# Kernel optimization log

Measured on AMD Instinct MI355X. Metric: run time of the kernel, lower is better.

The kernel has to match this reference:

```python
import jax, jax.numpy as jnp
import numpy as np

N_NODES = 50000
N_EDGES = 1600000
IN_DIM, HID_DIM, OUT_DIM = 512, 512, 256
K = 10        # APPNP propagation steps (num_layers)
ALPHA = 0.2   # teleport probability


def setup_inputs() -> dict:
    key = jax.random.key(0)
    ks = jax.random.split(key, 8)
    x = jax.random.normal(ks[0], (N_NODES, IN_DIM), dtype=jnp.float32)
    edge_index = jax.random.randint(ks[1], (2, N_EDGES), 0, N_NODES, dtype=jnp.int32)
    # Glorot-ish init for linear weights
    W1 = jax.random.normal(ks[2], (IN_DIM, HID_DIM), dtype=jnp.float32) / np.sqrt(IN_DIM)
    b1 = jnp.zeros((HID_DIM,), dtype=jnp.float32)
    W2 = jax.random.normal(ks[3], (HID_DIM, HID_DIM), dtype=jnp.float32) / np.sqrt(HID_DIM)
    b2 = jnp.zeros((HID_DIM,), dtype=jnp.float32)
    W3 = jax.random.normal(ks[4], (HID_DIM, OUT_DIM), dtype=jnp.float32) / np.sqrt(HID_DIM)
    b3 = jnp.zeros((OUT_DIM,), dtype=jnp.float32)
    return {"x": x, "edge_index": edge_index, "W1": W1, "b1": b1,
            "W2": W2, "b2": b2, "W3": W3, "b3": b3}


def reference(x, edge_index, W1, b1, W2, b2, W3, b3):
    n = x.shape[0]
    # MLP encoder (dropout is identity in inference mode)
    h = jax.nn.relu(x @ W1 + b1)
    h = jax.nn.relu(h @ W2 + b2)
    h = h @ W3 + b3
    # GCN symmetric normalization with self-loops (PyG gcn_norm)
    self_loops = jnp.arange(n, dtype=edge_index.dtype)
    src = jnp.concatenate([edge_index[0], self_loops])  # message sources j
    dst = jnp.concatenate([edge_index[1], self_loops])  # aggregation targets i
    deg = jax.ops.segment_sum(jnp.ones_like(src, dtype=h.dtype), dst, num_segments=n)
    dinv = jnp.where(deg > 0, jax.lax.rsqrt(jnp.maximum(deg, 1.0)), 0.0)
    norm = (dinv[src] * dinv[dst])[:, None]  # [E+N, 1]
    # APPNP: h <- (1-alpha) * A_hat @ h + alpha * h0, K times
    h0 = h
    for _ in range(K):
        agg = jax.ops.segment_sum(h[src] * norm, dst, num_segments=n)
        h = (1.0 - ALPHA) * agg + ALPHA * h0
    return h
```

## Files before the change

### kernel.cpp

```cpp
#include <hip/hip_runtime.h>
#include <hip/hip_bf16.h>
#include <stdint.h>

#define ALPHA_F 0.2f
#define K_STEPS 10

typedef __attribute__((ext_vector_type(8))) short short8;
typedef __attribute__((ext_vector_type(4))) float f32x4;
typedef __attribute__((ext_vector_type(4))) unsigned short u16x4;
typedef __attribute__((ext_vector_type(2))) int i32x2;

__device__ __forceinline__ float bf2f(unsigned short u) {
  union { unsigned int i; float f; } v; v.i = ((unsigned int)u) << 16; return v.f;
}
__device__ __forceinline__ unsigned short f2bf(float f) {
  unsigned int x = __float_as_uint(f);
  unsigned int r = (x + 0x7fffu + ((x >> 16) & 1u)) >> 16;
  return (unsigned short)r;
}

__device__ __forceinline__ void glds16(const void* g, void* l) {
  __builtin_amdgcn_global_load_lds(
      (const __attribute__((address_space(1))) void*)g,
      (__attribute__((address_space(3))) void*)l, 16, 0, 0);
}


__global__ void k_init_deg(int* __restrict__ deg, int n) {
  int i = blockIdx.x * blockDim.x + threadIdx.x;
  if (i < n) deg[i] = 1;
}

__global__ void k_hist(const int* __restrict__ dst, int* __restrict__ deg, int E) {
  int e = blockIdx.x * blockDim.x + threadIdx.x;
  if (e < E) atomicAdd(&deg[dst[e]], 1);
}

__global__ void k_scan(const int* __restrict__ counts, int* __restrict__ rowptr, int n) {
  __shared__ int tmp[1024];
  __shared__ int carry_s;
  const int tid = threadIdx.x;
  if (tid == 0) carry_s = 0;
  __syncthreads();
  for (int base = 0; base < n; base += 1024) {
    int idx = base + tid;
    int v = (idx < n) ? counts[idx] : 0;
    tmp[tid] = v;
    __syncthreads();
    #pragma unroll
    for (int off = 1; off < 1024; off <<= 1) {
      int t = (tid >= off) ? tmp[tid - off] : 0;
      __syncthreads();
      tmp[tid] += t;
      __syncthreads();
    }
    int c = carry_s;
    if (idx < n) rowptr[idx] = c + tmp[tid] - v;
    __syncthreads();
    if (tid == 0) carry_s = c + tmp[1023];
    __syncthreads();
  }
  if (tid == 0) rowptr[n] = carry_s;
}

__global__ void k_dinv_cursor(const int* __restrict__ deg, const int* __restrict__ rowptr,
                              float* __restrict__ dinv, int* __restrict__ cursor, int n) {
  int i = blockIdx.x * blockDim.x + threadIdx.x;
  if (i < n) {
    dinv[i] = 1.0f / sqrtf((float)deg[i]);
    cursor[i] = rowptr[i];
  }
}

__global__ void k_scatter(const int* __restrict__ src, const int* __restrict__ dst,
                          int* __restrict__ cursor, i32x2* __restrict__ edge,
                          const float* __restrict__ dinv, int E, int n) {
  int idx = blockIdx.x * blockDim.x + threadIdx.x;
  if (idx >= E + n) return;
  int s, d;
  if (idx < E) { s = src[idx]; d = dst[idx]; }
  else         { s = d = idx - E; }
  int pos = atomicAdd(&cursor[d], 1);
  i32x2 e;
  e.x = s;
  e.y = __float_as_int(dinv[s]);
  edge[pos] = e;
}


__global__ void k_f2b8(const float* __restrict__ src, unsigned short* __restrict__ dst,
                       int validRows, int cols, long total8) {
  long idx = (long)blockIdx.x * blockDim.x + threadIdx.x;
  if (idx >= total8) return;
  size_t base = (size_t)idx * 8;
  int row = (int)(base / (size_t)cols);
  uint4 o;
  if (row < validRows) {
    const float4 f0 = *reinterpret_cast<const float4*>(src + base);
    const float4 f1 = *reinterpret_cast<const float4*>(src + base + 4);
    o.x = f2bf(f0.x) | ((unsigned)f2bf(f0.y) << 16);
    o.y = f2bf(f0.z) | ((unsigned)f2bf(f0.w) << 16);
    o.z = f2bf(f1.x) | ((unsigned)f2bf(f1.y) << 16);
    o.w = f2bf(f1.z) | ((unsigned)f2bf(f1.w) << 16);
  } else {
    o = make_uint4(0, 0, 0, 0);
  }
  *reinterpret_cast<uint4*>(dst + base) = o;
}

__global__ void k_wtrans(const float* __restrict__ W, unsigned short* __restrict__ Wt,
                         int K, int Nw) {
  int idx = blockIdx.x * blockDim.x + threadIdx.x;
  if (idx >= K * Nw) return;
  int nn = idx / K, kk = idx - nn * K;
  Wt[(size_t)nn * K + kk] = f2bf(W[(size_t)kk * Nw + nn]);
}


template<bool OUT_BF16, bool RELU>
__global__ __launch_bounds__(256)
void k_gemm_mfma(const unsigned short* __restrict__ A,
                 const unsigned short* __restrict__ Bt,
                 const float* __restrict__ bias,
                 void* __restrict__ C, int Nn, int K) {
  __shared__ unsigned short As[128 * 32];
  __shared__ unsigned short Bs[128 * 32];
  const int tid = threadIdx.x;
  const int lane = tid & 63;
  const int wid = tid >> 6;
  const int wr = wid >> 1, wc = wid & 1;
  const int bm = blockIdx.y * 128;
  const int bn = blockIdx.x * 128;

  f32x4 acc[4][4];
  #pragma unroll
  for (int i = 0; i < 4; ++i)
    #pragma unroll
    for (int j = 0; j < 4; ++j) acc[i][j] = (f32x4)0.f;

  const int srow = tid >> 2;
  const int skg = (tid & 3) << 3;
  const unsigned short* Ag = A + (size_t)(bm + srow) * K + skg;
  const unsigned short* Bg = Bt + (size_t)(bn + srow) * K + skg;
  unsigned short* lA = As + (wid << 9);
  unsigned short* lB = Bs + (wid << 9);

  const int frow = lane & 15;
  const int fk = (lane >> 4) << 3;

  for (int k0 = 0; k0 < K; k0 += 32) {
    __syncthreads();
    glds16(Ag + k0, lA);
    glds16(Ag + (size_t)64 * K + k0, lA + 2048);
    glds16(Bg + k0, lB);
    glds16(Bg + (size_t)64 * K + k0, lB + 2048);
    __syncthreads();

    short8 af[4], bq[4];
    #pragma unroll
    for (int mi = 0; mi < 4; ++mi)
      af[mi] = *reinterpret_cast<const short8*>(&As[(wr * 64 + mi * 16 + frow) * 32 + fk]);
    #pragma unroll
    for (int ni = 0; ni < 4; ++ni)
      bq[ni] = *reinterpret_cast<const short8*>(&Bs[(wc * 64 + ni * 16 + frow) * 32 + fk]);
    #pragma unroll
    for (int mi = 0; mi < 4; ++mi)
      #pragma unroll
      for (int ni = 0; ni < 4; ++ni)
        acc[mi][ni] = __builtin_amdgcn_mfma_f32_16x16x32_bf16(af[mi], bq[ni], acc[mi][ni], 0, 0, 0);
  }

  const int r0 = bm + wr * 64;
  const int c0 = bn + wc * 64;
  #pragma unroll
  for (int ni = 0; ni < 4; ++ni) {
    const int c = c0 + ni * 16 + (lane & 15);
    const float bv = bias[c];
    #pragma unroll
    for (int mi = 0; mi < 4; ++mi) {
      #pragma unroll
      for (int r = 0; r < 4; ++r) {
        const int row = r0 + mi * 16 + ((lane >> 4) << 2) + r;
        float v = acc[mi][ni][r] + bv;
        if constexpr (RELU) v = fmaxf(v, 0.f);
        if constexpr (OUT_BF16)
          ((unsigned short*)C)[(size_t)row * Nn + c] = f2bf(v);
        else
          ((float*)C)[(size_t)row * Nn + c] = v;
      }
    }
  }
}

__global__ void k_h0state(const float* __restrict__ h0, unsigned short* __restrict__ st,
                          long total8) {
  long idx = (long)blockIdx.x * blockDim.x + threadIdx.x;
  if (idx >= total8) return;
  size_t base = (size_t)idx * 8;
  const float4 f0 = *reinterpret_cast<const float4*>(h0 + base);
  const float4 f1 = *reinterpret_cast<const float4*>(h0 + base + 4);
  uint4 o;
  o.x = f2bf(f0.x) | ((unsigned)f2bf(f0.y) << 16);
  o.y = f2bf(f0.z) | ((unsigned)f2bf(f0.w) << 16);
  o.z = f2bf(f1.x) | ((unsigned)f2bf(f1.y) << 16);
  o.w = f2bf(f1.z) | ((unsigned)f2bf(f1.w) << 16);
  *reinterpret_cast<uint4*>(st + base) = o;
}


template<bool FINAL>
__global__ __launch_bounds__(256)
void k_appnp_b16(const unsigned short* __restrict__ hprev,
                 const float* __restrict__ h0,
                 void* __restrict__ outp,
                 const int* __restrict__ rowptr,
                 const i32x2* __restrict__ edge,
                 const float* __restrict__ dinv, int n) {
  const int lane = threadIdx.x & 63;
  const int i = blockIdx.x * 4 + (threadIdx.x >> 6);
  if (i >= n) return;
  const int beg = rowptr[i];
  const int end = rowptr[i + 1];
  const int d = lane << 2;
  float a0 = 0.f, a1 = 0.f, a2 = 0.f, a3 = 0.f;
  int e = beg;
  for (; e + 4 <= end; e += 4) {
    const i32x2 e0 = __builtin_nontemporal_load(edge + e);
    const i32x2 e1 = __builtin_nontemporal_load(edge + e + 1);
    const i32x2 e2 = __builtin_nontemporal_load(edge + e + 2);
    const i32x2 e3 = __builtin_nontemporal_load(edge + e + 3);
    const float w0 = __int_as_float(e0.y), w1 = __int_as_float(e1.y);
    const float w2 = __int_as_float(e2.y), w3 = __int_as_float(e3.y);
    const u16x4 v0 = *reinterpret_cast<const u16x4*>(hprev + (size_t)e0.x * 256 + d);
    const u16x4 v1 = *reinterpret_cast<const u16x4*>(hprev + (size_t)e1.x * 256 + d);
    const u16x4 v2 = *reinterpret_cast<const u16x4*>(hprev + (size_t)e2.x * 256 + d);
    const u16x4 v3 = *reinterpret_cast<const u16x4*>(hprev + (size_t)e3.x * 256 + d);
    a0 += w0 * bf2f(v0.x) + w1 * bf2f(v1.x) + w2 * bf2f(v2.x) + w3 * bf2f(v3.x);
    a1 += w0 * bf2f(v0.y) + w1 * bf2f(v1.y) + w2 * bf2f(v2.y) + w3 * bf2f(v3.y);
    a2 += w0 * bf2f(v0.z) + w1 * bf2f(v1.z) + w2 * bf2f(v2.z) + w3 * bf2f(v3.z);
    a3 += w0 * bf2f(v0.w) + w1 * bf2f(v1.w) + w2 * bf2f(v2.w) + w3 * bf2f(v3.w);
  }
  for (; e < end; ++e) {
    const i32x2 ee = __builtin_nontemporal_load(edge + e);
    const float w = __int_as_float(ee.y);
    const u16x4 v = *reinterpret_cast<const u16x4*>(hprev + (size_t)ee.x * 256 + d);
    a0 += w * bf2f(v.x); a1 += w * bf2f(v.y); a2 += w * bf2f(v.z); a3 += w * bf2f(v.w);
  }
  const float s = (1.0f - ALPHA_F) * dinv[i];
  const f32x4 h0v = __builtin_nontemporal_load(
      reinterpret_cast<const f32x4*>(h0 + (size_t)i * 256 + d));
  const float o0 = s * a0 + ALPHA_F * h0v.x;
  const float o1 = s * a1 + ALPHA_F * h0v.y;
  const float o2 = s * a2 + ALPHA_F * h0v.z;
  const float o3 = s * a3 + ALPHA_F * h0v.w;
  if constexpr (FINAL) {
    f32x4 o; o.x = o0; o.y = o1; o.z = o2; o.w = o3;
    __builtin_nontemporal_store(o, reinterpret_cast<f32x4*>((float*)outp + (size_t)i * 256 + d));
  } else {
    u16x4 o;
    o.x = f2bf(o0); o.y = f2bf(o1); o.z = f2bf(o2); o.w = f2bf(o3);
    *reinterpret_cast<u16x4*>((unsigned short*)outp + (size_t)i * 256 + d) = o;
  }
}


extern "C" void kernel_launch(void* const* d_in, const int* in_sizes, int n_in,
                              void* d_out, int out_size, void* d_ws, size_t ws_size,
                              hipStream_t stream) {
  const float* x  = (const float*)d_in[0];
  const int*   ei = (const int*)d_in[1];
  const float* W1 = (const float*)d_in[2];
  const float* b1 = (const float*)d_in[3];
  const float* W2 = (const float*)d_in[4];
  const float* b2 = (const float*)d_in[5];
  const float* W3 = (const float*)d_in[6];
  const float* b3 = (const float*)d_in[7];

  const int HID  = in_sizes[3];
  const int IN   = in_sizes[2] / HID;
  const int OUTD = in_sizes[7];
  const int E    = in_sizes[1] / 2;
  const int N    = in_sizes[0] / IN;
  const int Mpad = (N + 127) & ~127;
  const int* src = ei;
  const int* dst = ei + E;

  char* ws = (char*)d_ws;
  size_t off = 0;
  auto alloc = [&](size_t bytes) {
    char* p = ws + off;
    off += (bytes + 255) & ~(size_t)255;
    return p;
  };
  char* R1 = alloc((size_t)Mpad * ((IN > HID) ? IN : HID) * 2);
  char* R2 = alloc((size_t)Mpad * HID * 2);
  char* R4 = alloc((size_t)Mpad * OUTD * 4);
  int*   deg    = (int*)alloc((size_t)N * 4);
  int*   rowptr = (int*)alloc((size_t)(N + 1) * 4);
  int*   cursor = (int*)alloc((size_t)N * 4);
  float* dinv   = (float*)alloc((size_t)N * 4);
  i32x2* edge   = (i32x2*)alloc((size_t)(E + N) * 8);
  unsigned short* W1t = (unsigned short*)alloc((size_t)IN * HID * 2);
  unsigned short* W2t = (unsigned short*)alloc((size_t)HID * HID * 2);
  unsigned short* W3t = (unsigned short*)alloc((size_t)HID * OUTD * 2);
  (void)ws_size; (void)n_in; (void)out_size;

  unsigned short* xb = (unsigned short*)R1;
  unsigned short* h1 = (unsigned short*)R2;
  unsigned short* h2 = (unsigned short*)R1;
  float* h0 = (float*)R4;
  unsigned short* stateA = (unsigned short*)R2;
  unsigned short* stateB = (unsigned short*)R1;

  k_init_deg<<<(N + 255) / 256, 256, 0, stream>>>(deg, N);
  k_hist<<<(E + 255) / 256, 256, 0, stream>>>(dst, deg, E);
  k_scan<<<1, 1024, 0, stream>>>(deg, rowptr, N);
  k_dinv_cursor<<<(N + 255) / 256, 256, 0, stream>>>(deg, rowptr, dinv, cursor, N);
  k_scatter<<<(E + N + 255) / 256, 256, 0, stream>>>(src, dst, cursor, edge, dinv, E, N);

  {
    long total8 = (long)Mpad * IN / 8;
    k_f2b8<<<(int)((total8 + 255) / 256), 256, 0, stream>>>(x, xb, N, IN, total8);
    k_wtrans<<<(IN * HID + 255) / 256, 256, 0, stream>>>(W1, W1t, IN, HID);
    k_wtrans<<<(HID * HID + 255) / 256, 256, 0, stream>>>(W2, W2t, HID, HID);
    k_wtrans<<<(HID * OUTD + 255) / 256, 256, 0, stream>>>(W3, W3t, HID, OUTD);
  }

  {
    dim3 blk(256);
    dim3 g1(HID / 128, Mpad / 128);
    k_gemm_mfma<true, true><<<g1, blk, 0, stream>>>(xb, W1t, b1, h1, HID, IN);
    k_gemm_mfma<true, true><<<g1, blk, 0, stream>>>(h1, W2t, b2, h2, HID, HID);
    dim3 g3(OUTD / 128, Mpad / 128);
    k_gemm_mfma<false, false><<<g3, blk, 0, stream>>>(h2, W3t, b3, h0, OUTD, HID);
  }

  {
    long total8 = (long)N * OUTD / 8;
    k_h0state<<<(int)((total8 + 255) / 256), 256, 0, stream>>>(h0, stateA, total8);
  }

  {
    const int nblk = (N + 3) / 4;
    const unsigned short* cur = stateA;
    for (int step = 0; step < K_STEPS - 1; ++step) {
      unsigned short* dbuf = (step % 2 == 0) ? stateB : stateA;
      k_appnp_b16<false><<<nblk, 256, 0, stream>>>(cur, h0, dbuf, rowptr, edge, dinv, N);
      cur = dbuf;
    }
    k_appnp_b16<true><<<nblk, 256, 0, stream>>>(cur, h0, d_out, rowptr, edge, dinv, N);
  }
}
```

Baseline: 1.662 ms.

## Parallelize degree scan, tile weight transpose, keep h0 in bf16, pipeline gathers

```diff
diff --git a/kernel.cpp b/kernel.cpp
--- a/kernel.cpp
+++ b/kernel.cpp
@@ -26,48 +26,52 @@
 }
 
 
-__global__ void k_init_deg(int* __restrict__ deg, int n) {
-  int i = blockIdx.x * blockDim.x + threadIdx.x;
-  if (i < n) deg[i] = 1;
-}
-
 __global__ void k_hist(const int* __restrict__ dst, int* __restrict__ deg, int E) {
   int e = blockIdx.x * blockDim.x + threadIdx.x;
   if (e < E) atomicAdd(&deg[dst[e]], 1);
 }
 
-__global__ void k_scan(const int* __restrict__ counts, int* __restrict__ rowptr, int n) {
-  __shared__ int tmp[1024];
-  __shared__ int carry_s;
+__global__ __launch_bounds__(1024)
+void k_scanA(const int* __restrict__ deg, int* __restrict__ rowptr,
+             int* __restrict__ bsum, int n) {
+  __shared__ int buf[2][1024];
   const int tid = threadIdx.x;
-  if (tid == 0) carry_s = 0;
+  const int gid = blockIdx.x * 1024 + tid;
+  int v = (gid < n) ? (deg[gid] + 1) : 0;
+  int sel = 0;
+  buf[0][tid] = v;
   __syncthreads();
-  for (int base = 0; base < n; base += 1024) {
-    int idx = base + tid;
-    int v = (idx < n) ? counts[idx] : 0;
-    tmp[tid] = v;
+  #pragma unroll
+  for (int off = 1; off < 1024; off <<= 1) {
+    int t = buf[sel][tid] + ((tid >= off) ? buf[sel][tid - off] : 0);
+    buf[sel ^ 1][tid] = t;
+    sel ^= 1;
     __syncthreads();
-    #pragma unroll
-    for (int off = 1; off < 1024; off <<= 1) {
-      int t = (tid >= off) ? tmp[tid - off] : 0;
-      __syncthreads();
-      tmp[tid] += t;
-      __syncthreads();
-    }
-    int c = carry_s;
-    if (idx < n) rowptr[idx] = c + tmp[tid] - v;
-    __syncthreads();
-    if (tid == 0) carry_s = c + tmp[1023];
-    __syncthreads();
-  }
-  if (tid == 0) rowptr[n] = carry_s;
+  }
+  if (gid < n) rowptr[gid] = buf[sel][tid] - v;
+  if (tid == 0) bsum[blockIdx.x] = buf[sel][1023];
+}
+
+__global__ void k_scanB(int* __restrict__ bsum, int nb) {
+  if (threadIdx.x == 0 && blockIdx.x == 0) {
+    int acc = 0;
+    for (int i = 0; i < nb; ++i) { int t = bsum[i]; bsum[i] = acc; acc += t; }
+    bsum[nb] = acc;
+  }
+}
+
+__global__ void k_scanC(int* __restrict__ rowptr, const int* __restrict__ bsum,
+                        int n, int nb) {
+  int gid = blockIdx.x * blockDim.x + threadIdx.x;
+  if (gid < n) rowptr[gid] += bsum[gid >> 10];
+  else if (gid == n) rowptr[n] = bsum[nb];
 }
 
 __global__ void k_dinv_cursor(const int* __restrict__ deg, const int* __restrict__ rowptr,
                               float* __restrict__ dinv, int* __restrict__ cursor, int n) {
   int i = blockIdx.x * blockDim.x + threadIdx.x;
   if (i < n) {
-    dinv[i] = 1.0f / sqrtf((float)deg[i]);
+    dinv[i] = 1.0f / sqrtf((float)(deg[i] + 1));
     cursor[i] = rowptr[i];
   }
 }
@@ -108,12 +112,21 @@
   *reinterpret_cast<uint4*>(dst + base) = o;
 }
 
-__global__ void k_wtrans(const float* __restrict__ W, unsigned short* __restrict__ Wt,
-                         int K, int Nw) {
-  int idx = blockIdx.x * blockDim.x + threadIdx.x;
-  if (idx >= K * Nw) return;
-  int nn = idx / K, kk = idx - nn * K;
-  Wt[(size_t)nn * K + kk] = f2bf(W[(size_t)kk * Nw + nn]);
+__global__ __launch_bounds__(256)
+void k_wtrans(const float* __restrict__ W, unsigned short* __restrict__ Wt,
+              int K, int Nw) {
+  __shared__ float tile[32][33];
+  const int bn = blockIdx.x * 32;
+  const int bk = blockIdx.y * 32;
+  const int tx = threadIdx.x & 31;
+  const int ty = threadIdx.x >> 5;
+  #pragma unroll
+  for (int r = 0; r < 32; r += 8)
+    tile[r + ty][tx] = W[(size_t)(bk + r + ty) * Nw + bn + tx];
+  __syncthreads();
+  #pragma unroll
+  for (int r = 0; r < 32; r += 8)
+    Wt[(size_t)(bn + r + ty) * K + bk + tx] = f2bf(tile[tx][r + ty]);
 }
 
 
@@ -192,26 +205,13 @@
   }
 }
 
-__global__ void k_h0state(const float* __restrict__ h0, unsigned short* __restrict__ st,
-                          long total8) {
-  long idx = (long)blockIdx.x * blockDim.x + threadIdx.x;
-  if (idx >= total8) return;
-  size_t base = (size_t)idx * 8;
-  const float4 f0 = *reinterpret_cast<const float4*>(h0 + base);
-  const float4 f1 = *reinterpret_cast<const float4*>(h0 + base + 4);
-  uint4 o;
-  o.x = f2bf(f0.x) | ((unsigned)f2bf(f0.y) << 16);
-  o.y = f2bf(f0.z) | ((unsigned)f2bf(f0.w) << 16);
-  o.z = f2bf(f1.x) | ((unsigned)f2bf(f1.y) << 16);
-  o.w = f2bf(f1.z) | ((unsigned)f2bf(f1.w) << 16);
-  *reinterpret_cast<uint4*>(st + base) = o;
-}
-
+
+#define NTLD(p) __builtin_nontemporal_load(p)
 
 template<bool FINAL>
 __global__ __launch_bounds__(256)
 void k_appnp_b16(const unsigned short* __restrict__ hprev,
-                 const float* __restrict__ h0,
+                 const unsigned short* __restrict__ h0b,
                  void* __restrict__ outp,
                  const int* __restrict__ rowptr,
                  const i32x2* __restrict__ edge,
@@ -223,36 +223,61 @@
   const int end = rowptr[i + 1];
   const int d = lane << 2;
   float a0 = 0.f, a1 = 0.f, a2 = 0.f, a3 = 0.f;
+
+  auto gat = [&](int j) -> u16x4 {
+    return *reinterpret_cast<const u16x4*>(hprev + (size_t)j * 256 + d);
+  };
+  auto accq = [&](float w, u16x4 v) {
+    a0 += w * bf2f(v.x); a1 += w * bf2f(v.y);
+    a2 += w * bf2f(v.z); a3 += w * bf2f(v.w);
+  };
+
+  const int quads = (end - beg) >> 2;
   int e = beg;
-  for (; e + 4 <= end; e += 4) {
-    const i32x2 e0 = __builtin_nontemporal_load(edge + e);
-    const i32x2 e1 = __builtin_nontemporal_load(edge + e + 1);
-    const i32x2 e2 = __builtin_nontemporal_load(edge + e + 2);
-    const i32x2 e3 = __builtin_nontemporal_load(edge + e + 3);
-    const float w0 = __int_as_float(e0.y), w1 = __int_as_float(e1.y);
-    const float w2 = __int_as_float(e2.y), w3 = __int_as_float(e3.y);
-    const u16x4 v0 = *reinterpret_cast<const u16x4*>(hprev + (size_t)e0.x * 256 + d);
-    const u16x4 v1 = *reinterpret_cast<const u16x4*>(hprev + (size_t)e1.x * 256 + d);
-    const u16x4 v2 = *reinterpret_cast<const u16x4*>(hprev + (size_t)e2.x * 256 + d);
-    const u16x4 v3 = *reinterpret_cast<const u16x4*>(hprev + (size_t)e3.x * 256 + d);
-    a0 += w0 * bf2f(v0.x) + w1 * bf2f(v1.x) + w2 * bf2f(v2.x) + w3 * bf2f(v3.x);
-    a1 += w0 * bf2f(v0.y) + w1 * bf2f(v1.y) + w2 * bf2f(v2.y) + w3 * bf2f(v3.y);
-    a2 += w0 * bf2f(v0.z) + w1 * bf2f(v1.z) + w2 * bf2f(v2.z) + w3 * bf2f(v3.z);
-    a3 += w0 * bf2f(v0.w) + w1 * bf2f(v1.w) + w2 * bf2f(v2.w) + w3 * bf2f(v3.w);
+  if (quads >= 2) {
+    i32x2 t0 = NTLD(edge + e),     t1 = NTLD(edge + e + 1);
+    i32x2 t2 = NTLD(edge + e + 2), t3 = NTLD(edge + e + 3);
+    i32x2 B0 = NTLD(edge + e + 4), B1 = NTLD(edge + e + 5);
+    i32x2 B2 = NTLD(edge + e + 6), B3 = NTLD(edge + e + 7);
+    u16x4 V0 = gat(t0.x), V1 = gat(t1.x), V2 = gat(t2.x), V3 = gat(t3.x);
+    float w0 = __int_as_float(t0.y), w1 = __int_as_float(t1.y);
+    float w2 = __int_as_float(t2.y), w3 = __int_as_float(t3.y);
+    for (int q = 2; q < quads; ++q) {
+      const i32x2* ep = edge + e + (q << 2);
+      const i32x2 C0 = NTLD(ep),     C1 = NTLD(ep + 1);
+      const i32x2 C2 = NTLD(ep + 2), C3 = NTLD(ep + 3);
+      const u16x4 U0 = gat(B0.x), U1 = gat(B1.x), U2 = gat(B2.x), U3 = gat(B3.x);
+      const float x0 = __int_as_float(B0.y), x1 = __int_as_float(B1.y);
+      const float x2 = __int_as_float(B2.y), x3 = __int_as_float(B3.y);
+      accq(w0, V0); accq(w1, V1); accq(w2, V2); accq(w3, V3);
+      V0 = U0; V1 = U1; V2 = U2; V3 = U3;
+      w0 = x0; w1 = x1; w2 = x2; w3 = x3;
+      B0 = C0; B1 = C1; B2 = C2; B3 = C3;
+    }
+    const u16x4 U0 = gat(B0.x), U1 = gat(B1.x), U2 = gat(B2.x), U3 = gat(B3.x);
+    accq(w0, V0); accq(w1, V1); accq(w2, V2); accq(w3, V3);
+    accq(__int_as_float(B0.y), U0); accq(__int_as_float(B1.y), U1);
+    accq(__int_as_float(B2.y), U2); accq(__int_as_float(B3.y), U3);
+    e += quads << 2;
+  } else if (quads == 1) {
+    const i32x2 t0 = NTLD(edge + e),     t1 = NTLD(edge + e + 1);
+    const i32x2 t2 = NTLD(edge + e + 2), t3 = NTLD(edge + e + 3);
+    const u16x4 V0 = gat(t0.x), V1 = gat(t1.x), V2 = gat(t2.x), V3 = gat(t3.x);
+    accq(__int_as_float(t0.y), V0); accq(__int_as_float(t1.y), V1);
+    accq(__int_as_float(t2.y), V2); accq(__int_as_float(t3.y), V3);
+    e += 4;
   }
   for (; e < end; ++e) {
-    const i32x2 ee = __builtin_nontemporal_load(edge + e);
-    const float w = __int_as_float(ee.y);
-    const u16x4 v = *reinterpret_cast<const u16x4*>(hprev + (size_t)ee.x * 256 + d);
-    a0 += w * bf2f(v.x); a1 += w * bf2f(v.y); a2 += w * bf2f(v.z); a3 += w * bf2f(v.w);
-  }
+    const i32x2 ee = NTLD(edge + e);
+    accq(__int_as_float(ee.y), gat(ee.x));
+  }
+
   const float s = (1.0f - ALPHA_F) * dinv[i];
-  const f32x4 h0v = __builtin_nontemporal_load(
-      reinterpret_cast<const f32x4*>(h0 + (size_t)i * 256 + d));
-  const float o0 = s * a0 + ALPHA_F * h0v.x;
-  const float o1 = s * a1 + ALPHA_F * h0v.y;
-  const float o2 = s * a2 + ALPHA_F * h0v.z;
-  const float o3 = s * a3 + ALPHA_F * h0v.w;
+  const u16x4 hv = NTLD(reinterpret_cast<const u16x4*>(h0b + (size_t)i * 256 + d));
+  const float o0 = s * a0 + ALPHA_F * bf2f(hv.x);
+  const float o1 = s * a1 + ALPHA_F * bf2f(hv.y);
+  const float o2 = s * a2 + ALPHA_F * bf2f(hv.z);
+  const float o3 = s * a3 + ALPHA_F * bf2f(hv.w);
   if constexpr (FINAL) {
     f32x4 o; o.x = o0; o.y = o1; o.z = o2; o.w = o3;
     __builtin_nontemporal_store(o, reinterpret_cast<f32x4*>((float*)outp + (size_t)i * 256 + d));
@@ -294,12 +319,13 @@
   };
   char* R1 = alloc((size_t)Mpad * ((IN > HID) ? IN : HID) * 2);
   char* R2 = alloc((size_t)Mpad * HID * 2);
-  char* R4 = alloc((size_t)Mpad * OUTD * 4);
+  char* R4 = alloc((size_t)Mpad * OUTD * 2);
   int*   deg    = (int*)alloc((size_t)N * 4);
   int*   rowptr = (int*)alloc((size_t)(N + 1) * 4);
   int*   cursor = (int*)alloc((size_t)N * 4);
   float* dinv   = (float*)alloc((size_t)N * 4);
-  i32x2* edge   = (i32x2*)alloc((size_t)(E + N) * 8);
+  int*   bsum   = (int*)alloc((size_t)256 * 4);
+  i32x2* edge   = (i32x2*)alloc((size_t)(E + N + 8) * 8);
   unsigned short* W1t = (unsigned short*)alloc((size_t)IN * HID * 2);
   unsigned short* W2t = (unsigned short*)alloc((size_t)HID * HID * 2);
   unsigned short* W3t = (unsigned short*)alloc((size_t)HID * OUTD * 2);
@@ -308,22 +334,26 @@
   unsigned short* xb = (unsigned short*)R1;
   unsigned short* h1 = (unsigned short*)R2;
   unsigned short* h2 = (unsigned short*)R1;
-  float* h0 = (float*)R4;
+  unsigned short* h0b = (unsigned short*)R4;
   unsigned short* stateA = (unsigned short*)R2;
   unsigned short* stateB = (unsigned short*)R1;
 
-  k_init_deg<<<(N + 255) / 256, 256, 0, stream>>>(deg, N);
+  hipMemsetAsync(deg, 0, (size_t)N * 4, stream);
   k_hist<<<(E + 255) / 256, 256, 0, stream>>>(dst, deg, E);
-  k_scan<<<1, 1024, 0, stream>>>(deg, rowptr, N);
+  const int nb = (N + 1023) / 1024;
+  k_scanA<<<nb, 1024, 0, stream>>>(deg, rowptr, bsum, N);
+  k_scanB<<<1, 64, 0, stream>>>(bsum, nb);
+  k_scanC<<<(N + 256) / 256, 256, 0, stream>>>(rowptr, bsum, N, nb);
   k_dinv_cursor<<<(N + 255) / 256, 256, 0, stream>>>(deg, rowptr, dinv, cursor, N);
   k_scatter<<<(E + N + 255) / 256, 256, 0, stream>>>(src, dst, cursor, edge, dinv, E, N);
 
   {
     long total8 = (long)Mpad * IN / 8;
     k_f2b8<<<(int)((total8 + 255) / 256), 256, 0, stream>>>(x, xb, N, IN, total8);
-    k_wtrans<<<(IN * HID + 255) / 256, 256, 0, stream>>>(W1, W1t, IN, HID);
-    k_wtrans<<<(HID * HID + 255) / 256, 256, 0, stream>>>(W2, W2t, HID, HID);
-    k_wtrans<<<(HID * OUTD + 255) / 256, 256, 0, stream>>>(W3, W3t, HID, OUTD);
+    dim3 tb(256);
+    k_wtrans<<<dim3(HID / 32, IN / 32), tb, 0, stream>>>(W1, W1t, IN, HID);
+    k_wtrans<<<dim3(HID / 32, HID / 32), tb, 0, stream>>>(W2, W2t, HID, HID);
+    k_wtrans<<<dim3(OUTD / 32, HID / 32), tb, 0, stream>>>(W3, W3t, HID, OUTD);
   }
 
   {
@@ -332,22 +362,17 @@
     k_gemm_mfma<true, true><<<g1, blk, 0, stream>>>(xb, W1t, b1, h1, HID, IN);
     k_gemm_mfma<true, true><<<g1, blk, 0, stream>>>(h1, W2t, b2, h2, HID, HID);
     dim3 g3(OUTD / 128, Mpad / 128);
-    k_gemm_mfma<false, false><<<g3, blk, 0, stream>>>(h2, W3t, b3, h0, OUTD, HID);
-  }
-
-  {
-    long total8 = (long)N * OUTD / 8;
-    k_h0state<<<(int)((total8 + 255) / 256), 256, 0, stream>>>(h0, stateA, total8);
+    k_gemm_mfma<true, false><<<g3, blk, 0, stream>>>(h2, W3t, b3, h0b, OUTD, HID);
   }
 
   {
     const int nblk = (N + 3) / 4;
-    const unsigned short* cur = stateA;
+    const unsigned short* cur = h0b;
     for (int step = 0; step < K_STEPS - 1; ++step) {
-      unsigned short* dbuf = (step % 2 == 0) ? stateB : stateA;
-      k_appnp_b16<false><<<nblk, 256, 0, stream>>>(cur, h0, dbuf, rowptr, edge, dinv, N);
+      unsigned short* dbuf = (step % 2 == 0) ? stateA : stateB;
+      k_appnp_b16<false><<<nblk, 256, 0, stream>>>(cur, h0b, dbuf, rowptr, edge, dinv, N);
       cur = dbuf;
     }
-    k_appnp_b16<true><<<nblk, 256, 0, stream>>>(cur, h0, d_out, rowptr, edge, dinv, N);
-  }
-}
+    k_appnp_b16<true><<<nblk, 256, 0, stream>>>(cur, h0b, d_out, rowptr, edge, dinv, N);
+  }
+}
```

After: 1.511 ms. 1.1x faster.
